# Kernel optimization log

Hardware: AMD Instinct MI355X
Metric: run time of the kernel (lower is better)

## Reference

```python
import jax, jax.numpy as jnp
import numpy as np

B, S, D, DO, L, E = 8, 2048, 256, 256, 8, 32768


def setup_inputs() -> dict:
    key = jax.random.key(0)
    k1, k2, k3, k4, k5, k6 = jax.random.split(key, 6)
    node_repr = jax.random.normal(k1, (B, S, D), dtype=jnp.float32)
    edge_src = jax.random.randint(k2, (B, E), 0, S, dtype=jnp.int32)
    edge_tgt = jax.random.randint(k3, (B, E), 0, S, dtype=jnp.int32)
    edge_label = jax.random.randint(k4, (B, E), 0, L, dtype=jnp.int32)
    # per-label Linear params (torch default: kaiming-ish uniform; values here are random stand-ins)
    bound = 1.0 / np.sqrt(D)
    W = jax.random.uniform(k5, (L, D, DO), dtype=jnp.float32, minval=-bound, maxval=bound)
    b = jax.random.uniform(k6, (L, DO), dtype=jnp.float32, minval=-bound, maxval=bound)
    return {"node_repr": node_repr, "edge_src": edge_src, "edge_tgt": edge_tgt,
            "edge_label": edge_label, "W": W, "b": b}


def reference(node_repr, edge_src, edge_tgt, edge_label, W, b):
    # Transform every node by every label's linear once: y[b,l,s,:] = x[b,s,:] @ W[l] + b[l]
    y = jnp.einsum('bsd,ldo->blso', node_repr, W) + b[None, :, None, :]  # [B,L,S,DO]
    bidx = jnp.arange(node_repr.shape[0])[:, None]                       # [B,1]
    msgs = y[bidx, edge_label, edge_src]                                 # [B,E,DO] gather
    out = jnp.zeros(node_repr.shape[:2] + (W.shape[-1],), dtype=node_repr.dtype)
    out = out.at[bidx, edge_tgt].add(msgs)                               # scatter-add into targets
    return jax.nn.relu(out)
```

## Files before the change

kernel.cpp:

```cpp
#include <hip/hip_runtime.h>
#include <stdint.h>

constexpr int NB = 8;
constexpr int NS = 2048;
constexpr int ND = 256;
constexpr int NDO = 256;
constexpr int NL = 8;
constexpr int NE = 32768;
constexpr int K2 = NL * ND;
constexpr int CAP = 32;

typedef __attribute__((ext_vector_type(8))) short bf16x8;
typedef __attribute__((ext_vector_type(4))) float f32x4;
typedef unsigned int u32;

__device__ __forceinline__ float bf2f(uint32_t u) {
    return __uint_as_float(u << 16);
}
__device__ __forceinline__ uint16_t f2bf(float f) {
    uint32_t x = __float_as_uint(f);
    uint32_t r = (x + 0x7fffu + ((x >> 16) & 1u)) >> 16;
    return (uint16_t)r;
}

__device__ __forceinline__ void gl_lds16(const void* gptr, void* lptr) {
    __builtin_amdgcn_global_load_lds(
        (const __attribute__((address_space(1))) u32*)gptr,
        (__attribute__((address_space(3))) u32*)lptr, 16, 0, 0);
}

__global__ __launch_bounds__(256) void part_kernel(
    const float* __restrict__ W, ushort* __restrict__ wt2,
    const int* __restrict__ esrc, const int* __restrict__ etgt,
    const int* __restrict__ elab,
    int* __restrict__ cursor, ushort* __restrict__ bucket) {
    int bid = blockIdx.x;
    int tid = threadIdx.x;
    if (bid < 1024) {
        int i = bid * 256 + tid;
        int b = i >> 15;
        int c = (b << 14) + etgt[i] * NL + elab[i];
        int p = atomicAdd(&cursor[c], 1);
        if (p < CAP) bucket[(size_t)c * CAP + p] = (ushort)esrc[i];
    } else {
        __shared__ float tile[64][65];
        int tb = bid - 1024;
        int kt = tb & 31, ot = tb >> 5;
        int k0 = kt * 64, o0 = ot * 64;
        int rr = tid >> 6;
        int cc = tid & 63;
        for (int r16 = 0; r16 < 16; r16++) {
            int row = r16 * 4 + rr;
            tile[row][cc] = W[(size_t)(k0 + row) * NDO + o0 + cc];
        }
        __syncthreads();
        for (int r16 = 0; r16 < 16; r16++) {
            int orow = r16 * 4 + rr;
            wt2[(size_t)(o0 + orow) * K2 + k0 + cc] = f2bf(tile[cc][orow]);
        }
    }
}

__global__ __launch_bounds__(256) void agg_kernel(
    const float* __restrict__ x, const float* __restrict__ bias,
    const int* __restrict__ cursor, const ushort* __restrict__ bucket,
    ushort* __restrict__ Z, ushort* __restrict__ bsum) {
    int bid = blockIdx.x;
    int b = bid & 7;
    int lane = threadIdx.x & 63;
    int t = (bid >> 3) * 4 + (threadIdx.x >> 6);
    int g = b * NS + t;

    int cv = (lane < 8) ? cursor[(g << 3) + lane] : 0;

    const ushort* bp = bucket + (size_t)g * (NL * CAP);
    int my[4];
#pragma unroll
    for (int c = 0; c < 4; c++) my[c] = bp[c * 64 + lane];

    const float4* x4 = (const float4*)x + (size_t)b * NS * 64;
    ushort* zrow = Z + (size_t)g * K2;

#pragma unroll
    for (int l = 0; l < 8; l++) {
        int n = __shfl(cv, l);
        if (n > CAP) n = CAP;
        float4 a; a.x = a.y = a.z = a.w = 0.f;
        for (int q = 0; q < n; q++) {
            int src = __shfl(my[l >> 1], (l & 1) * CAP + q);
            float4 xv = x4[(size_t)src * 64 + lane];
            a.x += xv.x; a.y += xv.y; a.z += xv.z; a.w += xv.w;
        }
        ushort4 ob;
        ob.x = f2bf(a.x); ob.y = f2bf(a.y); ob.z = f2bf(a.z); ob.w = f2bf(a.w);
        ((ushort4*)(zrow + l * ND))[lane] = ob;
    }

    float4 ab; ab.x = ab.y = ab.z = ab.w = 0.f;
#pragma unroll
    for (int l = 0; l < 8; l++) {
        float cf = (float)__shfl(cv, l);
        float4 bv = ((const float4*)bias)[l * 64 + lane];
        ab.x += cf * bv.x; ab.y += cf * bv.y; ab.z += cf * bv.z; ab.w += cf * bv.w;
    }
    ushort4 sb;
    sb.x = f2bf(ab.x); sb.y = f2bf(ab.y); sb.z = f2bf(ab.z); sb.w = f2bf(ab.w);
    ((ushort4*)(bsum + (size_t)g * NDO))[lane] = sb;
}

__global__ __launch_bounds__(256) void gemm2_kernel(
    const ushort* __restrict__ Z, const ushort* __restrict__ wt2,
    const ushort* __restrict__ bsum, float* __restrict__ out) {
    int wgid = (blockIdx.x & 7) * 64 + (blockIdx.x >> 3);
    int m0 = (wgid >> 1) * 64;
    int n0 = (wgid & 1) * 128;

    __shared__ ushort As[64 * 64];
    __shared__ ushort Bs[128 * 64];

    int tid = threadIdx.x;
    int lane = tid & 63;
    int wave = __builtin_amdgcn_readfirstlane(tid >> 6);
    int wm = wave & 1, wn = wave >> 1;
    int ln = lane & 15, quad = lane >> 4;

    f32x4 acc[2][4] = {};

    const ushort* Ag = Z + (size_t)m0 * K2;
    const ushort* Bg = wt2 + (size_t)n0 * K2;

    for (int k0 = 0; k0 < K2; k0 += 64) {
#pragma unroll
        for (int p = 0; p < 2; p++) {
            int cid = p * 256 + tid;
            int r = cid >> 3, ch = (cid & 7) ^ (r & 7);
            gl_lds16(Ag + (size_t)r * K2 + k0 + ch * 8, &As[(p * 256 + wave * 64) * 8]);
        }
#pragma unroll
        for (int p = 0; p < 4; p++) {
            int cid = p * 256 + tid;
            int r = cid >> 3, ch = (cid & 7) ^ (r & 7);
            gl_lds16(Bg + (size_t)r * K2 + k0 + ch * 8, &Bs[(p * 256 + wave * 64) * 8]);
        }
        __syncthreads();

        bf16x8 af[2][2], bfr[2][4];
#pragma unroll
        for (int ks = 0; ks < 2; ks++) {
#pragma unroll
            for (int i = 0; i < 2; i++) {
                int row = wm * 32 + i * 16 + ln;
                int ch = (ks * 4 + quad) ^ (row & 7);
                af[ks][i] = *(const bf16x8*)&As[row * 64 + ch * 8];
            }
#pragma unroll
            for (int j = 0; j < 4; j++) {
                int row = wn * 64 + j * 16 + ln;
                int ch = (ks * 4 + quad) ^ (row & 7);
                bfr[ks][j] = *(const bf16x8*)&Bs[row * 64 + ch * 8];
            }
        }
#pragma unroll
        for (int ks = 0; ks < 2; ks++)
            for (int i = 0; i < 2; i++)
                for (int j = 0; j < 4; j++)
                    acc[i][j] = __builtin_amdgcn_mfma_f32_16x16x32_bf16(
                        af[ks][i], bfr[ks][j], acc[i][j], 0, 0, 0);
        __syncthreads();
    }

    for (int j = 0; j < 4; j++) {
        int col = n0 + wn * 64 + j * 16 + ln;
        for (int i = 0; i < 2; i++) {
            int rbase = m0 + wm * 32 + i * 16 + quad * 4;
            for (int r = 0; r < 4; r++) {
                size_t idx = (size_t)(rbase + r) * NDO + col;
                float v = acc[i][j][r] + bf2f(bsum[idx]);
                out[idx] = fmaxf(v, 0.f);
            }
        }
    }
}

extern "C" void kernel_launch(void* const* d_in, const int* in_sizes, int n_in,
                              void* d_out, int out_size, void* d_ws, size_t ws_size,
                              hipStream_t stream) {
    const float* x    = (const float*)d_in[0];
    const int*   esrc = (const int*)d_in[1];
    const int*   etgt = (const int*)d_in[2];
    const int*   elab = (const int*)d_in[3];
    const float* W    = (const float*)d_in[4];
    const float* bias = (const float*)d_in[5];
    float* out = (float*)d_out;

    char* ws = (char*)d_ws;
    ushort* wt2    = (ushort*)(ws);
    int*    cursor = (int*)(ws + 1048576);
    ushort* bucket = (ushort*)(ws + 1572864);
    ushort* Z      = (ushort*)(ws + 10485760);
    ushort* bsum   = (ushort*)(ws + 77594624);

    hipMemsetAsync(cursor, 0, NB * NS * NL * sizeof(int), stream);
    part_kernel<<<1152, 256, 0, stream>>>(W, wt2, esrc, etgt, elab, cursor, bucket);
    agg_kernel<<<4096, 256, 0, stream>>>(x, bias, cursor, bucket, Z, bsum);
    gemm2_kernel<<<512, 256, 0, stream>>>(Z, wt2, bsum, out);
}
```

Baseline: 139.9 us.

## Fuse bias-count sum into GEMM epilogue and double GEMM K-tile

Removes the bsum intermediate: the aggregation kernel no longer computes count-weighted bias sums, and the GEMM epilogue instead loads per-row label counts and the bias slice into LDS and computes them in fp32. The GEMM K-tile grows from 64 to 128, halving the number of barrier-synchronised load iterations. This cuts a global write and read of the bias buffer, at the cost of more LDS per block, which may lower occupancy, and extra epilogue arithmetic.

```diff
diff --git a/kernel.cpp b/kernel.cpp
--- a/kernel.cpp
+++ b/kernel.cpp
@@ -62,9 +62,9 @@
 }
 
 __global__ __launch_bounds__(256) void agg_kernel(
-    const float* __restrict__ x, const float* __restrict__ bias,
+    const float* __restrict__ x,
     const int* __restrict__ cursor, const ushort* __restrict__ bucket,
-    ushort* __restrict__ Z, ushort* __restrict__ bsum) {
+    ushort* __restrict__ Z) {
     int bid = blockIdx.x;
     int b = bid & 7;
     int lane = threadIdx.x & 63;
@@ -95,28 +95,20 @@
         ob.x = f2bf(a.x); ob.y = f2bf(a.y); ob.z = f2bf(a.z); ob.w = f2bf(a.w);
         ((ushort4*)(zrow + l * ND))[lane] = ob;
     }
-
-    float4 ab; ab.x = ab.y = ab.z = ab.w = 0.f;
-#pragma unroll
-    for (int l = 0; l < 8; l++) {
-        float cf = (float)__shfl(cv, l);
-        float4 bv = ((const float4*)bias)[l * 64 + lane];
-        ab.x += cf * bv.x; ab.y += cf * bv.y; ab.z += cf * bv.z; ab.w += cf * bv.w;
-    }
-    ushort4 sb;
-    sb.x = f2bf(ab.x); sb.y = f2bf(ab.y); sb.z = f2bf(ab.z); sb.w = f2bf(ab.w);
-    ((ushort4*)(bsum + (size_t)g * NDO))[lane] = sb;
 }
 
 __global__ __launch_bounds__(256) void gemm2_kernel(
     const ushort* __restrict__ Z, const ushort* __restrict__ wt2,
-    const ushort* __restrict__ bsum, float* __restrict__ out) {
+    const int* __restrict__ cursor, const float* __restrict__ bias,
+    float* __restrict__ out) {
     int wgid = (blockIdx.x & 7) * 64 + (blockIdx.x >> 3);
     int m0 = (wgid >> 1) * 64;
     int n0 = (wgid & 1) * 128;
 
-    __shared__ ushort As[64 * 64];
-    __shared__ ushort Bs[128 * 64];
+    __shared__ ushort As[64 * 128];
+    __shared__ ushort Bs[128 * 128];
+    __shared__ int cnt_s[64 * 8];
+    __shared__ float bias_s[8 * 128];
 
     int tid = threadIdx.x;
     int lane = tid & 63;
@@ -124,59 +116,75 @@
     int wm = wave & 1, wn = wave >> 1;
     int ln = lane & 15, quad = lane >> 4;
 
+    {
+        int e = tid * 2;
+        *(int2*)&cnt_s[e] = *(const int2*)&cursor[(size_t)m0 * 8 + e];
+        int f = tid * 4;
+        int l = f >> 7, col = f & 127;
+        *(float4*)&bias_s[f] = *(const float4*)&bias[l * NDO + n0 + col];
+    }
+
     f32x4 acc[2][4] = {};
 
     const ushort* Ag = Z + (size_t)m0 * K2;
     const ushort* Bg = wt2 + (size_t)n0 * K2;
 
-    for (int k0 = 0; k0 < K2; k0 += 64) {
-#pragma unroll
-        for (int p = 0; p < 2; p++) {
-            int cid = p * 256 + tid;
-            int r = cid >> 3, ch = (cid & 7) ^ (r & 7);
-            gl_lds16(Ag + (size_t)r * K2 + k0 + ch * 8, &As[(p * 256 + wave * 64) * 8]);
-        }
+    for (int k0 = 0; k0 < K2; k0 += 128) {
 #pragma unroll
         for (int p = 0; p < 4; p++) {
             int cid = p * 256 + tid;
-            int r = cid >> 3, ch = (cid & 7) ^ (r & 7);
+            int r = cid >> 4, ch = (cid & 15) ^ (r & 7);
+            gl_lds16(Ag + (size_t)r * K2 + k0 + ch * 8, &As[(p * 256 + wave * 64) * 8]);
+        }
+#pragma unroll
+        for (int p = 0; p < 8; p++) {
+            int cid = p * 256 + tid;
+            int r = cid >> 4, ch = (cid & 15) ^ (r & 7);
             gl_lds16(Bg + (size_t)r * K2 + k0 + ch * 8, &Bs[(p * 256 + wave * 64) * 8]);
         }
         __syncthreads();
 
-        bf16x8 af[2][2], bfr[2][4];
-#pragma unroll
-        for (int ks = 0; ks < 2; ks++) {
+#pragma unroll
+        for (int ks = 0; ks < 4; ks++) {
+            bf16x8 af[2], bfr[4];
 #pragma unroll
             for (int i = 0; i < 2; i++) {
                 int row = wm * 32 + i * 16 + ln;
-                int ch = (ks * 4 + quad) ^ (row & 7);
-                af[ks][i] = *(const bf16x8*)&As[row * 64 + ch * 8];
+                int ci = (ks * 4 + quad) ^ (row & 7);
+                af[i] = *(const bf16x8*)&As[row * 128 + ci * 8];
             }
 #pragma unroll
             for (int j = 0; j < 4; j++) {
                 int row = wn * 64 + j * 16 + ln;
-                int ch = (ks * 4 + quad) ^ (row & 7);
-                bfr[ks][j] = *(const bf16x8*)&Bs[row * 64 + ch * 8];
+                int ci = (ks * 4 + quad) ^ (row & 7);
+                bfr[j] = *(const bf16x8*)&Bs[row * 128 + ci * 8];
             }
-        }
-#pragma unroll
-        for (int ks = 0; ks < 2; ks++)
+#pragma unroll
             for (int i = 0; i < 2; i++)
+#pragma unroll
                 for (int j = 0; j < 4; j++)
                     acc[i][j] = __builtin_amdgcn_mfma_f32_16x16x32_bf16(
-                        af[ks][i], bfr[ks][j], acc[i][j], 0, 0, 0);
+                        af[i], bfr[j], acc[i][j], 0, 0, 0);
+        }
         __syncthreads();
     }
 
-    for (int j = 0; j < 4; j++) {
-        int col = n0 + wn * 64 + j * 16 + ln;
-        for (int i = 0; i < 2; i++) {
-            int rbase = m0 + wm * 32 + i * 16 + quad * 4;
-            for (int r = 0; r < 4; r++) {
-                size_t idx = (size_t)(rbase + r) * NDO + col;
-                float v = acc[i][j][r] + bf2f(bsum[idx]);
-                out[idx] = fmaxf(v, 0.f);
+#pragma unroll
+    for (int i = 0; i < 2; i++) {
+#pragma unroll
+        for (int r = 0; r < 4; r++) {
+            int row_l = wm * 32 + i * 16 + quad * 4 + r;
+            float cw[8];
+#pragma unroll
+            for (int l = 0; l < 8; l++) cw[l] = (float)cnt_s[row_l * 8 + l];
+#pragma unroll
+            for (int j = 0; j < 4; j++) {
+                int col_l = wn * 64 + j * 16 + ln;
+                float bs = 0.f;
+#pragma unroll
+                for (int l = 0; l < 8; l++) bs += cw[l] * bias_s[l * 128 + col_l];
+                float v = acc[i][j][r] + bs;
+                out[(size_t)(m0 + row_l) * NDO + n0 + col_l] = fmaxf(v, 0.f);
             }
         }
     }
@@ -198,10 +206,9 @@
     int*    cursor = (int*)(ws + 1048576);
     ushort* bucket = (ushort*)(ws + 1572864);
     ushort* Z      = (ushort*)(ws + 10485760);
-    ushort* bsum   = (ushort*)(ws + 77594624);
 
     hipMemsetAsync(cursor, 0, NB * NS * NL * sizeof(int), stream);
     part_kernel<<<1152, 256, 0, stream>>>(W, wt2, esrc, etgt, elab, cursor, bucket);
-    agg_kernel<<<4096, 256, 0, stream>>>(x, bias, cursor, bucket, Z, bsum);
-    gemm2_kernel<<<512, 256, 0, stream>>>(Z, wt2, bsum, out);
-}
+    agg_kernel<<<4096, 256, 0, stream>>>(x, cursor, bucket, Z);
+    gemm2_kernel<<<512, 256, 0, stream>>>(Z, wt2, cursor, bias, out);
+}
```

After: 161.1 us. 15.1% more time.
